# Performance work log

Measured on AMD Instinct MI355X. Metric: run time of the kernel, lower is better.

## Reference

```python
import jax, jax.numpy as jnp
import numpy as np

N = 200000      # active voxels
INC = 64
OUTC = 128
G = 128         # voxel grid extent
K = 27          # 3^3 kernel offsets
EPS = 1e-5


def setup_inputs() -> dict:
    rng = np.random.default_rng(0)
    # sample N unique occupied voxels on a G^3 grid
    lin = rng.choice(G ** 3, size=N, replace=False)
    coords = np.stack([lin // (G * G), (lin // G) % G, lin % G], axis=1).astype(np.int64)
    # dense lookup table (padded by 1) mapping voxel -> row index, -1 if empty
    Gp = G + 2
    lut = np.full(Gp ** 3, -1, dtype=np.int64)
    c = coords + 1
    lut[c[:, 0] * Gp * Gp + c[:, 1] * Gp + c[:, 2]] = np.arange(N)
    # neighbor map for all 27 offsets (kmap of the submanifold sparse conv)
    offs = np.array([[dx, dy, dz] for dx in (-1, 0, 1) for dy in (-1, 0, 1) for dz in (-1, 0, 1)], dtype=np.int64)
    nmap = np.empty((K, N), dtype=np.int64)
    for k in range(K):
        cc = c + offs[k]
        nmap[k] = lut[cc[:, 0] * Gp * Gp + cc[:, 1] * Gp + cc[:, 2]]

    key = jax.random.key(0)
    k1, k2, k3, k4 = jax.random.split(key, 4)
    feats = jax.random.normal(k1, (N, INC), jnp.float32)
    # kaiming-ish scale for the 27 per-offset weight matrices
    weight = jax.random.normal(k2, (K, INC, OUTC), jnp.float32) * (1.0 / np.sqrt(K * INC))
    gamma = jax.random.uniform(k3, (OUTC,), jnp.float32, 0.5, 1.5)
    beta = jax.random.normal(k4, (OUTC,), jnp.float32) * 0.1
    return {"feats": feats, "weight": weight, "gamma": gamma, "beta": beta,
            "neighbor_map": jnp.asarray(nmap)}


def reference(feats, weight, gamma, beta, neighbor_map):
    # Sparse submanifold 3D conv: for each kernel offset, gather neighbor
    # features (masked where no neighbor exists) and accumulate GEMMs.
    n = feats.shape[0]
    outc = weight.shape[2]

    def body(acc, xs):
        idx, w = xs                                   # idx: [N], w: [INC,OUTC]
        g = jnp.where((idx >= 0)[:, None], feats[jnp.clip(idx, 0)], 0.0)  # [N,INC]
        return acc + g @ w, None

    out, _ = jax.lax.scan(body, jnp.zeros((n, outc), feats.dtype),
                          (neighbor_map, weight))
    # BatchNorm (training-mode batch stats over points) + ReLU
    mean = out.mean(axis=0)
    var = out.var(axis=0)
    out = (out - mean) * jax.lax.rsqrt(var + EPS) * gamma + beta
    return jax.nn.relu(out)
```

## Files before the change

### kernel.cpp

```cpp
#include <hip/hip_runtime.h>
#include <hip/hip_bf16.h>

#define NPTS 200000
#define INC  64
#define OUTC 128
#define KTAP 27
#define EPSV 1e-5f
#define BM   128
#define NSHADOW 32

typedef __attribute__((ext_vector_type(8))) short bf16x8;
typedef __attribute__((ext_vector_type(4))) float f32x4;

__device__ __forceinline__ unsigned short f2bf(float f) {
  unsigned int u = __float_as_uint(f);
  return (unsigned short)((u + 0x7FFFu + ((u >> 16) & 1u)) >> 16);
}

__global__ void prep_wfrag(const float* __restrict__ w, unsigned char* __restrict__ img) {
  int tap = blockIdx.x;
  const float* wk = w + tap * (INC * OUTC);
  for (int id = threadIdx.x; id < 1024; id += blockDim.x) {
    int lane = id & 63;
    int ck   = id >> 6;
    int ct   = ck >> 1, kk = ck & 1;
    int c    = ct * 16 + (lane & 15);
    int k0   = kk * 32 + (lane >> 4) * 8;
    ushort4 lo, hi;
    lo.x = f2bf(wk[(k0+0)*OUTC + c]); lo.y = f2bf(wk[(k0+1)*OUTC + c]);
    lo.z = f2bf(wk[(k0+2)*OUTC + c]); lo.w = f2bf(wk[(k0+3)*OUTC + c]);
    hi.x = f2bf(wk[(k0+4)*OUTC + c]); hi.y = f2bf(wk[(k0+5)*OUTC + c]);
    hi.z = f2bf(wk[(k0+6)*OUTC + c]); hi.w = f2bf(wk[(k0+7)*OUTC + c]);
    unsigned char* d = img + (size_t)tap * 16384 + (size_t)id * 16;
    *(ushort4*)d       = lo;
    *(ushort4*)(d + 8) = hi;
  }
}

__global__ __launch_bounds__(256) void prep_feats(const float* __restrict__ f,
                                                  unsigned short* __restrict__ o) {
  size_t i = (size_t)blockIdx.x * 256 + threadIdx.x;
  float4 a = ((const float4*)f)[i * 2];
  float4 b = ((const float4*)f)[i * 2 + 1];
  ushort4 ha = make_ushort4(f2bf(a.x), f2bf(a.y), f2bf(a.z), f2bf(a.w));
  ushort4 hb = make_ushort4(f2bf(b.x), f2bf(b.y), f2bf(b.z), f2bf(b.w));
  ((ushort4*)o)[i * 2]     = ha;
  ((ushort4*)o)[i * 2 + 1] = hb;
}

__global__ __launch_bounds__(512, 4) void conv_main(
    const unsigned short* __restrict__ fbf,
    const int*   __restrict__ nmap,
    const unsigned char* __restrict__ wimg,
    float* __restrict__ out,
    float* __restrict__ shadow)
{
  __shared__ __align__(16) unsigned char ldsB[2][16384];

  const int t    = threadIdx.x;
  const int lane = t & 63;
  const int w    = t >> 6;
  const int cg   = w & 1;
  const int rg   = w >> 1;
  const int n0   = blockIdx.x * BM;
  const int l15  = lane & 15;
  const int lg   = lane >> 4;

  f32x4 zv = {0.f, 0.f, 0.f, 0.f};
  f32x4 acc[2][4];
  #pragma unroll
  for (int i = 0; i < 2; ++i)
    #pragma unroll
    for (int j = 0; j < 4; ++j) acc[i][j] = zv;

  const int nr0 = n0 + rg * 32 + l15;
  const int nr1 = nr0 + 16;
  const bool ok0 = nr0 < NPTS, ok1 = nr1 < NPTS;
  const int nc0 = ok0 ? nr0 : (NPTS - 1);
  const int nc1 = ok1 ? nr1 : (NPTS - 1);

  const unsigned char* fbp = (const unsigned char*)fbf;
  auto gp = [&](int g, bool ok) -> const unsigned char* {
    int gc = (g >= 0) ? g : NPTS;
    gc = ok ? gc : NPTS;
    return fbp + (size_t)gc * 128 + lg * 16;
  };

  auto stage = [&](int k, int slot) {
    const unsigned char* src = wimg + (size_t)k * 16384 + (size_t)t * 16;
    __builtin_amdgcn_global_load_lds(
        (const __attribute__((address_space(1))) void*)src,
        (__attribute__((address_space(3))) void*)(&ldsB[slot][t * 16]), 16, 0, 0);
    __builtin_amdgcn_global_load_lds(
        (const __attribute__((address_space(1))) void*)(src + 8192),
        (__attribute__((address_space(3))) void*)(&ldsB[slot][t * 16 + 8192]), 16, 0, 0);
  };

  const unsigned bb = (unsigned)(cg * 8192 + lane * 16);

  auto compute = [&](int slot, bf16x8& A0, bf16x8& A1, bf16x8& A2, bf16x8& A3) {
    const unsigned char* bufR = ldsB[slot];
    #pragma unroll
    for (int kk = 0; kk < 2; ++kk) {
      bf16x8 b0 = *(const bf16x8*)(bufR + bb + kk * 1024 + 0 * 2048);
      bf16x8 b1 = *(const bf16x8*)(bufR + bb + kk * 1024 + 1 * 2048);
      bf16x8 b2 = *(const bf16x8*)(bufR + bb + kk * 1024 + 2 * 2048);
      bf16x8 b3 = *(const bf16x8*)(bufR + bb + kk * 1024 + 3 * 2048);
      bf16x8 a0 = kk ? A1 : A0;
      bf16x8 a1 = kk ? A3 : A2;
      acc[0][0] = __builtin_amdgcn_mfma_f32_16x16x32_bf16(a0, b0, acc[0][0], 0, 0, 0);
      acc[0][1] = __builtin_amdgcn_mfma_f32_16x16x32_bf16(a0, b1, acc[0][1], 0, 0, 0);
      acc[0][2] = __builtin_amdgcn_mfma_f32_16x16x32_bf16(a0, b2, acc[0][2], 0, 0, 0);
      acc[0][3] = __builtin_amdgcn_mfma_f32_16x16x32_bf16(a0, b3, acc[0][3], 0, 0, 0);
      acc[1][0] = __builtin_amdgcn_mfma_f32_16x16x32_bf16(a1, b0, acc[1][0], 0, 0, 0);
      acc[1][1] = __builtin_amdgcn_mfma_f32_16x16x32_bf16(a1, b1, acc[1][1], 0, 0, 0);
      acc[1][2] = __builtin_amdgcn_mfma_f32_16x16x32_bf16(a1, b2, acc[1][2], 0, 0, 0);
      acc[1][3] = __builtin_amdgcn_mfma_f32_16x16x32_bf16(a1, b3, acc[1][3], 0, 0, 0);
    }
  };

  auto do_tap = [&](int kn, int slot,
                    bf16x8& A0, bf16x8& A1, bf16x8& A2, bf16x8& A3,
                    int& Q0, int& Q1) {
    int knx = (kn + 1 < KTAP) ? (kn + 1) : (KTAP - 1);
    stage(knx, slot ^ 1);
    __builtin_amdgcn_sched_barrier(0);
    const unsigned char* p0 = gp(Q0, ok0);
    const unsigned char* p1 = gp(Q1, ok1);
    bf16x8 nA0 = *(const bf16x8*)p0;
    bf16x8 nA1 = *(const bf16x8*)(p0 + 64);
    bf16x8 nA2 = *(const bf16x8*)p1;
    bf16x8 nA3 = *(const bf16x8*)(p1 + 64);
    int kq = (kn + 4 < KTAP) ? (kn + 4) : (KTAP - 1);
    int nQ0 = nmap[(size_t)kq * NPTS + nc0];
    int nQ1 = nmap[(size_t)kq * NPTS + nc1];
    __builtin_amdgcn_sched_barrier(0);
    compute(slot, A0, A1, A2, A3);
    A0 = nA0; A1 = nA1; A2 = nA2; A3 = nA3;
    Q0 = nQ0; Q1 = nQ1;
    asm volatile("s_waitcnt vmcnt(6)" ::: "memory");
    asm volatile("s_waitcnt lgkmcnt(0)" ::: "memory");
    __builtin_amdgcn_s_barrier();
    __builtin_amdgcn_sched_barrier(0);
  };

  int j00 = nmap[nc0],                     j01 = nmap[nc1];
  int j10 = nmap[(size_t)NPTS + nc0],      j11 = nmap[(size_t)NPTS + nc1];
  int q00 = nmap[(size_t)2 * NPTS + nc0],  q01 = nmap[(size_t)2 * NPTS + nc1];
  int q10 = nmap[(size_t)3 * NPTS + nc0],  q11 = nmap[(size_t)3 * NPTS + nc1];

  bf16x8 aC0, aC1, aC2, aC3;
  bf16x8 aN0, aN1, aN2, aN3;
  { const unsigned char* p = gp(j00, ok0); aC0 = *(const bf16x8*)p; aC1 = *(const bf16x8*)(p + 64); }
  { const unsigned char* p = gp(j01, ok1); aC2 = *(const bf16x8*)p; aC3 = *(const bf16x8*)(p + 64); }
  { const unsigned char* p = gp(j10, ok0); aN0 = *(const bf16x8*)p; aN1 = *(const bf16x8*)(p + 64); }
  { const unsigned char* p = gp(j11, ok1); aN2 = *(const bf16x8*)p; aN3 = *(const bf16x8*)(p + 64); }

  stage(0, 0);
  asm volatile("s_waitcnt vmcnt(0)" ::: "memory");
  asm volatile("s_waitcnt lgkmcnt(0)" ::: "memory");
  __builtin_amdgcn_s_barrier();
  __builtin_amdgcn_sched_barrier(0);

  #pragma unroll 1
  for (int kn = 0; kn < KTAP - 1; kn += 2) {
    do_tap(kn,     0, aC0, aC1, aC2, aC3, q00, q01);
    do_tap(kn + 1, 1, aN0, aN1, aN2, aN3, q10, q11);
  }
  compute(0, aC0, aC1, aC2, aC3);

  float* mysh = shadow + (blockIdx.x & (NSHADOW - 1)) * 256;
  #pragma unroll
  for (int nf = 0; nf < 4; ++nf) {
    int c = cg * 64 + nf * 16 + l15;
    float s = 0.f, s2 = 0.f;
    #pragma unroll
    for (int rt = 0; rt < 2; ++rt) {
      #pragma unroll
      for (int r = 0; r < 4; ++r) {
        float v = acc[rt][nf][r];
        int n = n0 + rg * 32 + rt * 16 + lg * 4 + r;
        if (n < NPTS) {
          s += v; s2 += v * v;
          out[(size_t)n * OUTC + c] = v;
        }
      }
    }
    s  += __shfl_xor(s, 16);  s  += __shfl_xor(s, 32);
    s2 += __shfl_xor(s2, 16); s2 += __shfl_xor(s2, 32);
    if (lane < 16) {
      atomicAdd(&mysh[c], s);
      atomicAdd(&mysh[128 + c], s2);
    }
  }
}

__global__ void finalize_stats(const float* __restrict__ shadow,
                               const float* __restrict__ gamma,
                               const float* __restrict__ beta,
                               float* __restrict__ scale,
                               float* __restrict__ shift) {
  __shared__ float accs[256];
  int t = threadIdx.x;
  float s = 0.f;
  for (int b = 0; b < NSHADOW; ++b) s += shadow[b * 256 + t];
  accs[t] = s;
  __syncthreads();
  if (t < OUTC) {
    float mean = accs[t] * (1.0f / (float)NPTS);
    float var  = accs[128 + t] * (1.0f / (float)NPTS) - mean * mean;
    var = fmaxf(var, 0.f);
    float sc = gamma[t] * rsqrtf(var + EPSV);
    scale[t] = sc;
    shift[t] = beta[t] - mean * sc;
  }
}

__global__ __launch_bounds__(256) void norm_relu(float* __restrict__ out,
                                                 const float* __restrict__ scale,
                                                 const float* __restrict__ shift) {
  __shared__ float s_sc[OUTC], s_sh[OUTC];
  if (threadIdx.x < OUTC) {
    s_sc[threadIdx.x] = scale[threadIdx.x];
    s_sh[threadIdx.x] = shift[threadIdx.x];
  }
  __syncthreads();
  const long total = (long)NPTS * OUTC / 4;
  for (long i = (long)blockIdx.x * blockDim.x + threadIdx.x; i < total;
       i += (long)gridDim.x * blockDim.x) {
    float4 v = ((float4*)out)[i];
    int cb = (int)(i & 31) * 4;
    v.x = fmaxf(v.x * s_sc[cb + 0] + s_sh[cb + 0], 0.f);
    v.y = fmaxf(v.y * s_sc[cb + 1] + s_sh[cb + 1], 0.f);
    v.z = fmaxf(v.z * s_sc[cb + 2] + s_sh[cb + 2], 0.f);
    v.w = fmaxf(v.w * s_sc[cb + 3] + s_sh[cb + 3], 0.f);
    ((float4*)out)[i] = v;
  }
}

extern "C" void kernel_launch(void* const* d_in, const int* in_sizes, int n_in,
                              void* d_out, int out_size, void* d_ws, size_t ws_size,
                              hipStream_t stream) {
  (void)in_sizes; (void)n_in; (void)out_size; (void)ws_size;
  const float* feats  = (const float*)d_in[0];
  const float* weight = (const float*)d_in[1];
  const float* gamma  = (const float*)d_in[2];
  const float* beta   = (const float*)d_in[3];
  const int*   nmap   = (const int*)d_in[4];
  float* out = (float*)d_out;

  unsigned char* ws = (unsigned char*)d_ws;
  const size_t FBF_BYTES  = (size_t)(NPTS + 1) * 128;
  const size_t WIMG_BYTES = (size_t)KTAP * 16384;
  unsigned short* fbf = (unsigned short*)ws;
  unsigned char* wimg = ws + FBF_BYTES;
  float* shadow = (float*)(ws + FBF_BYTES + WIMG_BYTES);
  float* scale  = shadow + NSHADOW * 256;
  float* shift  = scale + 128;

  hipMemsetAsync(shadow, 0, NSHADOW * 256 * sizeof(float), stream);
  hipMemsetAsync(fbf + (size_t)NPTS * 64, 0, 128, stream);
  prep_wfrag<<<KTAP, 256, 0, stream>>>(weight, wimg);
  prep_feats<<<6250, 256, 0, stream>>>(feats, fbf);
  int grid = (NPTS + BM - 1) / BM;
  conv_main<<<grid, 512, 0, stream>>>(fbf, nmap, wimg, out, shadow);
  finalize_stats<<<1, 256, 0, stream>>>(shadow, gamma, beta, scale, shift);
  norm_relu<<<4096, 256, 0, stream>>>(out, scale, shift);
}
```

Measured before the change: 169.1 us.

## Replace per-tap block barriers with LDS flag-based producer/consumer weight ring

```diff
diff --git a/kernel.cpp b/kernel.cpp
--- a/kernel.cpp
+++ b/kernel.cpp
@@ -55,7 +55,9 @@
     float* __restrict__ out,
     float* __restrict__ shadow)
 {
-  __shared__ __align__(16) unsigned char ldsB[2][16384];
+  __shared__ __align__(16) unsigned char ldsB[4][16384];
+  __shared__ int rdy_[4];
+  __shared__ int done_[4];
 
   const int t    = threadIdx.x;
   const int lane = t & 63;
@@ -86,20 +88,10 @@
     return fbp + (size_t)gc * 128 + lg * 16;
   };
 
-  auto stage = [&](int k, int slot) {
-    const unsigned char* src = wimg + (size_t)k * 16384 + (size_t)t * 16;
-    __builtin_amdgcn_global_load_lds(
-        (const __attribute__((address_space(1))) void*)src,
-        (__attribute__((address_space(3))) void*)(&ldsB[slot][t * 16]), 16, 0, 0);
-    __builtin_amdgcn_global_load_lds(
-        (const __attribute__((address_space(1))) void*)(src + 8192),
-        (__attribute__((address_space(3))) void*)(&ldsB[slot][t * 16 + 8192]), 16, 0, 0);
-  };
-
   const unsigned bb = (unsigned)(cg * 8192 + lane * 16);
 
   auto compute = [&](int slot, bf16x8& A0, bf16x8& A1, bf16x8& A2, bf16x8& A3) {
-    const unsigned char* bufR = ldsB[slot];
+    const unsigned char* bufR = &ldsB[0][0] + (size_t)slot * 16384;
     #pragma unroll
     for (int kk = 0; kk < 2; ++kk) {
       bf16x8 b0 = *(const bf16x8*)(bufR + bb + kk * 1024 + 0 * 2048);
@@ -119,12 +111,36 @@
     }
   };
 
-  auto do_tap = [&](int kn, int slot,
-                    bf16x8& A0, bf16x8& A1, bf16x8& A2, bf16x8& A3,
-                    int& Q0, int& Q1) {
-    int knx = (kn + 1 < KTAP) ? (kn + 1) : (KTAP - 1);
-    stage(knx, slot ^ 1);
+  int kpw = w;
+
+  auto duty = [&](int kn) {
+    if (kpw < KTAP && kpw <= kn + 3) {
+      int ss = kpw & 3, g = kpw >> 2;
+      while (*(volatile int*)&done_[ss] != 8 * g) __builtin_amdgcn_s_sleep(1);
+      const unsigned char* src = wimg + (size_t)kpw * 16384 + (size_t)lane * 16;
+      unsigned char* dst = &ldsB[ss][lane * 16];
+      #pragma unroll
+      for (int j = 0; j < 16; ++j)
+        __builtin_amdgcn_global_load_lds(
+            (const __attribute__((address_space(1))) void*)(src + j * 1024),
+            (__attribute__((address_space(3))) void*)(dst + j * 1024), 16, 0, 0);
+      asm volatile("s_waitcnt vmcnt(0)" ::: "memory");
+      if (lane == 0) *(volatile int*)&rdy_[ss] = kpw;
+      kpw += 8;
+    }
+    while (*(volatile int*)&rdy_[kn & 3] != kn) __builtin_amdgcn_s_sleep(1);
+    asm volatile("" ::: "memory");
     __builtin_amdgcn_sched_barrier(0);
+  };
+  auto consumed = [&](int kn) {
+    asm volatile("s_waitcnt lgkmcnt(0)" ::: "memory");
+    asm volatile("" ::: "memory");
+    if (lane == 0) atomicAdd(&done_[kn & 3], 1);
+  };
+
+  auto tap_body = [&](int kn,
+                      bf16x8& A0, bf16x8& A1, bf16x8& A2, bf16x8& A3,
+                      int& Q0, int& Q1) {
     const unsigned char* p0 = gp(Q0, ok0);
     const unsigned char* p1 = gp(Q1, ok1);
     bf16x8 nA0 = *(const bf16x8*)p0;
@@ -135,14 +151,12 @@
     int nQ0 = nmap[(size_t)kq * NPTS + nc0];
     int nQ1 = nmap[(size_t)kq * NPTS + nc1];
     __builtin_amdgcn_sched_barrier(0);
-    compute(slot, A0, A1, A2, A3);
+    compute(kn & 3, A0, A1, A2, A3);
     A0 = nA0; A1 = nA1; A2 = nA2; A3 = nA3;
     Q0 = nQ0; Q1 = nQ1;
-    asm volatile("s_waitcnt vmcnt(6)" ::: "memory");
-    asm volatile("s_waitcnt lgkmcnt(0)" ::: "memory");
-    __builtin_amdgcn_s_barrier();
-    __builtin_amdgcn_sched_barrier(0);
-  };
+  };
+
+  if (t < 4) { rdy_[t] = -1; done_[t] = 0; }
 
   int j00 = nmap[nc0],                     j01 = nmap[nc1];
   int j10 = nmap[(size_t)NPTS + nc0],      j11 = nmap[(size_t)NPTS + nc1];
@@ -156,18 +170,19 @@
   { const unsigned char* p = gp(j10, ok0); aN0 = *(const bf16x8*)p; aN1 = *(const bf16x8*)(p + 64); }
   { const unsigned char* p = gp(j11, ok1); aN2 = *(const bf16x8*)p; aN3 = *(const bf16x8*)(p + 64); }
 
-  stage(0, 0);
-  asm volatile("s_waitcnt vmcnt(0)" ::: "memory");
-  asm volatile("s_waitcnt lgkmcnt(0)" ::: "memory");
-  __builtin_amdgcn_s_barrier();
-  __builtin_amdgcn_sched_barrier(0);
+  __syncthreads();
 
   #pragma unroll 1
   for (int kn = 0; kn < KTAP - 1; kn += 2) {
-    do_tap(kn,     0, aC0, aC1, aC2, aC3, q00, q01);
-    do_tap(kn + 1, 1, aN0, aN1, aN2, aN3, q10, q11);
-  }
-  compute(0, aC0, aC1, aC2, aC3);
+    duty(kn);
+    tap_body(kn, aC0, aC1, aC2, aC3, q00, q01);
+    consumed(kn);
+    duty(kn + 1);
+    tap_body(kn + 1, aN0, aN1, aN2, aN3, q10, q11);
+    consumed(kn + 1);
+  }
+  duty(KTAP - 1);
+  compute((KTAP - 1) & 3, aC0, aC1, aC2, aC3);
 
   float* mysh = shadow + (blockIdx.x & (NSHADOW - 1)) * 256;
   #pragma unroll
```

Result: slower. 200.3 us (+18.5%).
